# Optimization experiments

Hardware: AMD Instinct MI355X
Metric: run time of the kernel (lower is better)

The kernel has to match this reference:

```python
import jax, jax.numpy as jnp
import numpy as np

LS = (0, 1, 2)
DIMS = tuple(2 * l + 1 for l in LS)          # (1, 3, 5)
MULS = (128, 64, 32)                          # node irreps multiplicities (= attention*heads)
ATT_MULS = (16, 8, 4)                         # attention_irreps multiplicities per head
N_HEADS = 8
N_IRREPS_ATT = sum(ATT_MULS)                  # 28
ATTN_NORM = 1.0 / np.sqrt(N_IRREPS_ATT)
CG = tuple(1.0 / np.sqrt(d) for d in DIMS)    # l (x) l -> 0e Clebsch-Gordan coefficient
N_NODES = 512
EDGE_ATTR_DIM = 32
NODE_DIM = sum(m * d for m, d in zip(MULS, DIMS))  # 480


def split_irreps(x, muls):
    """Split last axis into per-l blocks [..., mul_l, 2l+1]."""
    out, i = [], 0
    for mul, d in zip(muls, DIMS):
        out.append(x[..., i:i + mul * d].reshape(x.shape[:-1] + (mul, d)))
        i += mul * d
    return out


def merge_irreps(parts):
    return jnp.concatenate([p.reshape(p.shape[:-2] + (-1,)) for p in parts], axis=-1)


def e3_linear(parts, Ws):
    # equivariant linear: mixes multiplicities within each l, 1/sqrt(mul_in) norm
    return [jnp.einsum('nim,io->nom', p, W) / np.sqrt(p.shape[-2])
            for p, W in zip(parts, Ws)]


def setup_inputs() -> dict:
    key = jax.random.key(0)
    ks = jax.random.split(key, 16)
    inp = {
        'node_feat': jax.random.normal(ks[0], (N_NODES, NODE_DIM), jnp.float32),
        'edge_attr': jax.random.normal(ks[1], (N_NODES, N_NODES, EDGE_ATTR_DIM), jnp.float32),
        'edge_sh':   jax.random.normal(ks[2], (N_NODES, N_NODES, sum(DIMS)), jnp.float32),
    }
    i = 3
    for nm in ('Wq', 'Wk', 'Wv'):
        for l, mul in enumerate(MULS):
            inp[f'{nm}{l}'] = jax.random.normal(ks[i], (mul, mul), jnp.float32)
            i += 1
    inp['mW1'] = jax.random.normal(ks[i], (EDGE_ATTR_DIM + 2 * sum(MULS), 64), jnp.float32) * 0.05
    inp['mb1'] = jnp.zeros((64,), jnp.float32)
    inp['mW2'] = jax.random.normal(ks[i + 1], (64, 64), jnp.float32) * 0.1
    inp['mb2'] = jnp.zeros((64,), jnp.float32)
    inp['mW3'] = jax.random.normal(ks[i + 2], (64, N_HEADS), jnp.float32) * 0.1
    inp['mb3'] = jnp.zeros((N_HEADS,), jnp.float32)
    return inp


def reference(node_feat, edge_attr, edge_sh,
              Wq0, Wq1, Wq2, Wk0, Wk1, Wk2, Wv0, Wv1, Wv2,
              mW1, mb1, mW2, mb2, mW3, mb3):
    N = node_feat.shape[0]
    nf = split_irreps(node_feat, MULS)                 # per-l: [N, mul_l, 2l+1]
    sh = split_irreps(edge_sh, (1, 1, 1))              # per-l: [N, N, 1, 2l+1]

    def to_heads(parts):
        return [p.reshape(N, N_HEADS, am, d) for p, am, d in zip(parts, ATT_MULS, DIMS)]

    q = to_heads(e3_linear(nf, (Wq0, Wq1, Wq2)))
    k = to_heads(e3_linear(nf, (Wk0, Wk1, Wk2)))
    v = to_heads(e3_linear(nf, (Wv0, Wv1, Wv2)))

    # node (x) edge_sh -> scalars (0e): same-l inner products, CG = 1/sqrt(2l+1)
    feat_rec = jnp.concatenate(
        [jnp.einsum('rim,rsm->rsi', p, s[..., 0, :]) * c for p, s, c in zip(nf, sh, CG)], axis=-1)
    feat_snd = jnp.concatenate(
        [jnp.einsum('sim,rsm->rsi', p, s[..., 0, :]) * c for p, s, c in zip(nf, sh, CG)], axis=-1)
    edge_feat = jnp.concatenate([edge_attr, feat_rec, feat_snd], axis=-1)  # [N,N,480]

    h = jnp.tanh(edge_feat @ mW1 + mb1)
    h = jnp.tanh(h @ mW2 + mb2)
    edge_weight = h @ mW3 + mb3                        # [N, N, H]

    # elementwise q (x) k -> 0e, summed over irreps (== scaled dot product per head)
    logits = sum(jnp.einsum('rhim,shim->rsh', qp, kp) * c
                 for qp, kp, c in zip(q, k, CG))       # [N, N, H]
    weight = jax.nn.softmax(logits * ATTN_NORM + edge_weight, axis=-2)  # softmax over senders

    # weighted aggregation over senders, per irrep
    upd = [jnp.einsum('rsh,shim->rhim', weight, vp) for vp in v]
    # axis_to_mul: [N, H, mul, d] -> [N, H*mul, d]
    upd = [u.reshape(N, N_HEADS * am, d) for u, am, d in zip(upd, ATT_MULS, DIMS)]

    return node_feat + merge_irreps(upd)               # residual (irreps match)
```

## Files before the change

### kernel.cpp

```cpp
#include <hip/hip_runtime.h>
#include <hip/hip_bf16.h>
#include <stdint.h>


#define NNODES 512
#define NDIM   480

#define QG_OFF    0u
#define W2B_OFF   131072u
#define W3B_OFF   133120u
#define W1B_OFF   133632u
#define KG_OFF    245760u
#define VT_OFF    491520u
#define ARE_OFF   737280u
#define ASN_OFF   884736u
#define WF_OFF    1032192u
#define FLAG_OFF  1040384u
#define L_OFF     1040448u
#define WTQ_OFF   3137600u
#define WTK_OFF   3159104u
#define WTV_OFF   3180608u
#define W1T_OFF   3202112u

typedef float f32x4 __attribute__((ext_vector_type(4)));
typedef short s16x8 __attribute__((ext_vector_type(8)));

__device__ __forceinline__ float bf2f(uint16_t u) {
    return __uint_as_float(((uint32_t)u) << 16);
}
__device__ __forceinline__ uint16_t f2bf(float f) {
    union { __hip_bfloat16 h; uint16_t u; } cv;
    cv.h = __float2bfloat16(f);
    return cv.u;
}
__device__ __forceinline__ uint32_t packbf(float lo, float hi) {
    return ((uint32_t)f2bf(hi) << 16) | (uint32_t)f2bf(lo);
}
__device__ __forceinline__ float ldin(const void* p, size_t i, int f32) {
    return f32 ? ((const float*)p)[i] : bf2f(((const uint16_t*)p)[i]);
}
__device__ __forceinline__ float ftanh(float x) {
    float e = __builtin_amdgcn_exp2f(x * 2.885390081777927f);
    return 1.0f - 2.0f * __builtin_amdgcn_rcpf(e + 1.0f);
}

#define NS 16384
__global__ __launch_bounds__(256) void kW(
    const void* __restrict__ mW1, const void* __restrict__ mb1,
    const void* __restrict__ mW2, const void* __restrict__ mb2,
    const void* __restrict__ mW3, const void* __restrict__ mb3,
    const void* __restrict__ Wq0, const void* __restrict__ Wq1, const void* __restrict__ Wq2,
    const void* __restrict__ Wk0, const void* __restrict__ Wk1, const void* __restrict__ Wk2,
    const void* __restrict__ Wv0, const void* __restrict__ Wv1, const void* __restrict__ Wv2,
    float* __restrict__ ws, const void* __restrict__ nfu, int* __restrict__ flagp)
{
    __shared__ int sflag;
    const int t = threadIdx.x;
    if (t < 64) {
        uint32_t x = ((const uint32_t*)nfu)[64 + t];
        int e = (x >> 7) & 0xff;
        int good = (x != 0u) && (e >= 100) && (e <= 140);
        unsigned long long m = __ballot(good);
        if (t == 0) sflag = (__popcll(m) < 32) ? 1 : 0;
    }
    __syncthreads();
    const int f32 = sflag;
    if (blockIdx.x == 0 && t == 0) flagp[0] = f32;

    const int gt = blockIdx.x * 256 + t;
    float* Wf = ws + WF_OFF;

    for (int i = gt; i < 2048; i += NS) Wf[i] = ldin(mW1, i, f32);
    for (int i = gt; i < 64; i += NS) Wf[6656 + i] = ldin(mb1, i, f32);
    for (int i = gt; i < 64; i += NS) Wf[6720 + i] = ldin(mb2, i, f32);
    for (int i = gt; i < 8; i += NS)  Wf[6784 + i] = ldin(mb3, i, f32);

    {
        uint32_t* W2B = (uint32_t*)(ws + W2B_OFF);
        for (int i = gt; i < 2048; i += NS) {
            int f = i >> 8, lane = (i >> 2) & 63, w = i & 3;
            int nt = f >> 1, ks = f & 1, nl2 = lane & 15, gg = lane >> 4;
            int n = nt * 16 + nl2, kb = ks * 32 + gg * 8 + 2 * w;
            float lo = ldin(mW2, (size_t)kb * 64 + n, f32);
            float hi = ldin(mW2, (size_t)(kb + 1) * 64 + n, f32);
            W2B[i] = packbf(lo, hi);
        }
        uint32_t* W3B = (uint32_t*)(ws + W3B_OFF);
        for (int i = gt; i < 512; i += NS) {
            int ks = i >> 8, lane = (i >> 2) & 63, w = i & 3;
            int nl2 = lane & 15, gg = lane >> 4;
            int kb = ks * 32 + gg * 8 + 2 * w;
            float lo = (nl2 < 8) ? ldin(mW3, (size_t)kb * 8 + nl2, f32) : 0.f;
            float hi = (nl2 < 8) ? ldin(mW3, (size_t)(kb + 1) * 8 + nl2, f32) : 0.f;
            W3B[i] = packbf(lo, hi);
        }
        uint32_t* W1B = (uint32_t*)(ws + W1B_OFF);
        for (int i = gt; i < 1024; i += NS) {
            int nt = i >> 8, lane = (i >> 2) & 63, w = i & 3;
            int nl2 = lane & 15, gg = lane >> 4;
            int n = nt * 16 + nl2, k0 = gg * 8 + 2 * w;
            W1B[i] = packbf(ldin(mW1, (size_t)k0 * 64 + n, f32),
                            ldin(mW1, (size_t)(k0 + 1) * 64 + n, f32));
        }
    }

    const float e3n0 = 0.08838834764831845f, e3n1 = 0.125f, e3n2 = 0.17677669529663687f;
    const float cg1 = 0.5773502691896258f, cg2 = 0.4472135954999579f;
    const float attn = 0.1889822365046136f;

    const void* Wsrc[9] = {Wq0, Wq1, Wq2, Wk0, Wk1, Wk2, Wv0, Wv1, Wv2};
    float* Wdst[3] = {ws + WTQ_OFF, ws + WTK_OFF, ws + WTV_OFF};
    for (int kind = 0; kind < 3; ++kind) {
        const float f0 = (kind == 0) ? e3n0 * attn : e3n0;
        const float f1 = (kind == 0) ? e3n1 * cg1 * attn : e3n1;
        const float f2 = (kind == 0) ? e3n2 * cg2 * attn : e3n2;
        for (int i = gt; i < 16384; i += NS) {
            int o = i >> 7, ii = i & 127;
            Wdst[kind][i] = ldin(Wsrc[kind * 3], (size_t)ii * 128 + o, f32) * f0;
        }
        for (int i = gt; i < 4096; i += NS) {
            int o = i >> 6, ii = i & 63;
            Wdst[kind][16384 + i] = ldin(Wsrc[kind * 3 + 1], (size_t)ii * 64 + o, f32) * f1;
        }
        for (int i = gt; i < 1024; i += NS) {
            int o = i >> 5, ii = i & 31;
            Wdst[kind][20480 + i] = ldin(Wsrc[kind * 3 + 2], (size_t)ii * 32 + o, f32) * f2;
        }
    }
    float* W1T = ws + W1T_OFF;
    for (int i = gt; i < 30720; i += NS) {
        int o = i / 480, row = i - o * 480;
        float cgv;
        if (row < 160)      cgv = 1.0f;
        else if (row < 224) cgv = cg1;
        else if (row < 256) cgv = cg2;
        else if (row < 384) cgv = 1.0f;
        else if (row < 448) cgv = cg1;
        else                cgv = cg2;
        W1T[i] = ldin(mW1, (size_t)row * 64 + o, f32) * cgv;
    }
}

__global__ __launch_bounds__(256) void kA(
    const void* __restrict__ nfu,
    const float* __restrict__ WtQ, const float* __restrict__ WtK,
    const float* __restrict__ WtV, const float* __restrict__ W1T,
    uint32_t* __restrict__ qG, uint32_t* __restrict__ kG, uint16_t* __restrict__ vT,
    uint32_t* __restrict__ ArecG, uint32_t* __restrict__ AsndG,
    const int* __restrict__ flagp)
{
    const int f32 = flagp[0];
    const int n = blockIdx.x, t = threadIdx.x;
    __shared__ float nfs[480];
    for (int i = t; i < 480; i += 256) nfs[i] = ldin(nfu, (size_t)n * 480 + i, f32);

    if (t < 96) {
        const int kind3 = t >> 5, hh = (t >> 2) & 7, j = 60 + (t & 3);
        if (kind3 < 2) {
            const int row = n & 15, rt = n >> 4;
            const int cc = (j >> 3) ^ (n & 7);
            uint16_t* dst = (uint16_t*)(kind3 == 0 ? qG : kG);
            dst[((((size_t)rt * 8 + hh) * 16 + row) * 8 + cc) * 8 + (j & 7)] = 0;
        } else {
            vT[((size_t)(hh * 64 + j)) * 512 + n] = 0;
        }
    }
    __syncthreads();

    for (int idx = t; idx < 1440; idx += 256) {
        int kind = idx / 480, rem = idx - kind * 480;
        int o, m, mul, d, off, am, qoff, sub;
        if (rem < 128)      { o = rem;           m = 0;          mul = 128; d = 1; off = 0;   am = 16; qoff = 0;  sub = 0; }
        else if (rem < 320) { int x = rem - 128; o = x / 3; m = x - o * 3; mul = 64;  d = 3; off = 128; am = 8;  qoff = 16; sub = 16384; }
        else                { int x = rem - 320; o = x / 5; m = x - o * 5; mul = 32;  d = 5; off = 320; am = 4;  qoff = 40; sub = 20480; }
        const float* base = (kind == 0) ? WtQ : (kind == 1) ? WtK : WtV;
        const float4* W4 = reinterpret_cast<const float4*>(base + sub + o * mul);
        const float* nf0 = nfs + off + m;
        float ax = 0.f, ay = 0.f, az = 0.f, aw = 0.f;
        const int n4 = mul >> 2;
        for (int i4 = 0; i4 < n4; ++i4) {
            float4 w = W4[i4];
            int ib = 4 * i4 * d;
            ax += nf0[ib]         * w.x;
            ay += nf0[ib + d]     * w.y;
            az += nf0[ib + 2 * d] * w.z;
            aw += nf0[ib + 3 * d] * w.w;
        }
        float acc = (ax + ay) + (az + aw);
        int hh = o / am, a = o - hh * am;
        int j = qoff + a * d + m;
        if (kind == 2) {
            vT[((size_t)(hh * 64 + j)) * 512 + n] = f2bf(acc);
        } else {
            const int row = n & 15, rt = n >> 4;
            const int cc = (j >> 3) ^ (n & 7);
            uint16_t* dst = (uint16_t*)(kind == 0 ? qG : kG);
            dst[((((size_t)rt * 8 + hh) * 16 + row) * 8 + cc) * 8 + (j & 7)] = f2bf(acc);
        }
    }

    if (t < 128) {
        const int src = t >> 6, o = t & 63;
        float a[9];
        #pragma unroll
        for (int mi = 0; mi < 9; ++mi) {
            const int l = (mi == 0) ? 0 : (mi < 4 ? 1 : 2);
            const int m = (mi == 0) ? 0 : (mi < 4 ? mi - 1 : mi - 4);
            const int mul = (l == 0 ? 128 : l == 1 ? 64 : 32);
            const int d = 2 * l + 1;
            const int off = (l == 0 ? 0 : l == 1 ? 128 : 320);
            const int base = (src == 0) ? (l == 0 ? 32 : l == 1 ? 160 : 224)
                                        : (l == 0 ? 256 : l == 1 ? 384 : 448);
            const float4* W4 = reinterpret_cast<const float4*>(W1T + o * 480 + base);
            const float* nf0 = nfs + off + m;
            float ax = 0.f, ay = 0.f, az = 0.f, aw = 0.f;
            const int n4 = mul >> 2;
            for (int i4 = 0; i4 < n4; ++i4) {
                float4 w = W4[i4];
                int ib = 4 * i4 * d;
                ax += nf0[ib]         * w.x;
                ay += nf0[ib + d]     * w.y;
                az += nf0[ib + 2 * d] * w.z;
                aw += nf0[ib + 3 * d] * w.w;
            }
            a[mi] = (ax + ay) + (az + aw);
        }
        float b[9];
        #pragma unroll
        for (int mi = 0; mi < 9; ++mi) b[mi] = __shfl_xor(a[mi], 1, 64);
        if ((o & 1) == 0) {
            uint32_t* dst = (src ? AsndG : ArecG) + (size_t)n * 288 + (o >> 1);
            #pragma unroll
            for (int mi = 0; mi < 9; ++mi)
                dst[mi * 32] = ((uint32_t)f2bf(b[mi]) << 16) | (uint32_t)f2bf(a[mi]);
        }
    }
}

__global__ __launch_bounds__(256, 4) void kB(
    const void* __restrict__ eaG, const void* __restrict__ shG,
    const uint32_t* __restrict__ ArecG, const uint32_t* __restrict__ AsndG,
    const uint32_t* __restrict__ qG, const uint32_t* __restrict__ kG,
    const uint32_t* __restrict__ W2B, const uint32_t* __restrict__ W3B,
    const uint32_t* __restrict__ W1B,
    const float* __restrict__ Wf, float* __restrict__ L,
    const int* __restrict__ flagp)
{
    __shared__ __align__(16) uint32_t smem[10240];
    uint32_t* ArecS = smem;
    uint32_t* AsndS = smem + 4672;
    float* ewS = (float*)(smem + 8192);
    const int f32 = flagp[0];
    const int t = threadIdx.x;
    const int s0 = blockIdx.x * 16, r0 = blockIdx.y * 16;
    const int lane = t & 63, wv = t >> 6;
    const int g = lane >> 4, nl = lane & 15;

    const int rl = t >> 4, sl = t & 15;
    const int r = r0 + rl, s = s0 + sl;
    const size_t eidx = (((size_t)r) << 9) + s;

    uint32_t eaR[16];
    if (f32) {
        const float4* ep = reinterpret_cast<const float4*>((const float*)eaG + eidx * 32);
        #pragma unroll
        for (int i = 0; i < 8; ++i) {
            float4 v = ep[i];
            eaR[2 * i]     = ((uint32_t)f2bf(v.y) << 16) | (uint32_t)f2bf(v.x);
            eaR[2 * i + 1] = ((uint32_t)f2bf(v.w) << 16) | (uint32_t)f2bf(v.z);
        }
    } else {
        const uint4* ep = reinterpret_cast<const uint4*>((const uint32_t*)eaG + eidx * 16);
        #pragma unroll
        for (int i = 0; i < 4; ++i) {
            uint4 v = ep[i];
            eaR[4 * i] = v.x; eaR[4 * i + 1] = v.y; eaR[4 * i + 2] = v.z; eaR[4 * i + 3] = v.w;
        }
    }

    float sh0, sh1, sh2, sh3, sh4, sh5, sh6, sh7, sh8;
    {
        const size_t sb = eidx * 9;
        if (f32) {
            const float* shp = (const float*)shG + sb;
            sh0 = shp[0]; sh1 = shp[1]; sh2 = shp[2]; sh3 = shp[3]; sh4 = shp[4];
            sh5 = shp[5]; sh6 = shp[6]; sh7 = shp[7]; sh8 = shp[8];
        } else {
            const uint16_t* shp = (const uint16_t*)shG + sb;
            sh0 = bf2f(shp[0]); sh1 = bf2f(shp[1]); sh2 = bf2f(shp[2]);
            sh3 = bf2f(shp[3]); sh4 = bf2f(shp[4]); sh5 = bf2f(shp[5]);
            sh6 = bf2f(shp[6]); sh7 = bf2f(shp[7]); sh8 = bf2f(shp[8]);
        }
    }

    {
        s16x8 w1f[4];
        #pragma unroll
        for (int nt = 0; nt < 4; ++nt) w1f[nt] = ((const s16x8*)W1B)[nt * 64 + lane];
        uint16_t* sm16 = (uint16_t*)smem;
        #pragma unroll
        for (int mm = 0; mm < 4; ++mm) {
            const int srcl = mm * 16 + nl;
            uint32_t af0 = 0, af1 = 0, af2 = 0, af3 = 0;
            #pragma unroll
            for (int c = 0; c < 16; ++c) {
                const uint32_t tmp = (uint32_t)__shfl((int)eaR[c], srcl, 64);
                if ((c >> 2) == g) {
                    if ((c & 3) == 0)      af0 = tmp;
                    else if ((c & 3) == 1) af1 = tmp;
                    else if ((c & 3) == 2) af2 = tmp;
                    else                   af3 = tmp;
                }
            }
            union { uint32_t u[4]; s16x8 v; } afc;
            afc.u[0] = af0; afc.u[1] = af1; afc.u[2] = af2; afc.u[3] = af3;
            const s16x8 afrag = afc.v;
            const int mt = wv * 4 + mm;
            #pragma unroll
            for (int nt = 0; nt < 4; ++nt) {
                f32x4 a = {0.f, 0.f, 0.f, 0.f};
                a = __builtin_amdgcn_mfma_f32_16x16x32_bf16(afrag, w1f[nt], a, 0, 0, 0);
                #pragma unroll
                for (int rg = 0; rg < 4; ++rg) {
                    const int e = mt * 16 + g * 4 + rg;
                    const int o = nt * 16 + nl;
                    sm16[e * 64 + (((o >> 3) ^ (e & 7)) << 3) + (o & 7)] = f2bf(a[rg]);
                }
            }
        }
    }

    float h[64];
    #pragma unroll
    for (int c = 0; c < 8; ++c) {
        const int cc = c ^ (t & 7);
        const uint4 p = *(const uint4*)&smem[t * 32 + cc * 4];
        h[c * 8 + 0] = __uint_as_float(p.x << 16);
        h[c * 8 + 1] = __uint_as_float(p.x & 0xffff0000u);
        h[c * 8 + 2] = __uint_as_float(p.y << 16);
        h[c * 8 + 3] = __uint_as_float(p.y & 0xffff0000u);
        h[c * 8 + 4] = __uint_as_float(p.z << 16);
        h[c * 8 + 5] = __uint_as_float(p.z & 0xffff0000u);
        h[c * 8 + 6] = __uint_as_float(p.w << 16);
        h[c * 8 + 7] = __uint_as_float(p.w & 0xffff0000u);
    }
    #pragma unroll
    for (int o = 0; o < 64; ++o) h[o] += Wf[6656 + o];

    __syncthreads();

    for (int i = t; i < 16 * 288; i += 256) {
        int row = i / 288, c = i - row * 288;
        ArecS[row * 292 + c] = ArecG[(size_t)(r0 + row) * 288 + c];
        AsndS[row * 292 + c] = AsndG[(size_t)(s0 + row) * 288 + c];
    }
    __syncthreads();

    {
        const int rb = rl * 292, sb = sl * 292;
        #pragma unroll 1
        for (int mi = 0; mi < 9; ++mi) {
            float shv = sh0;
            shv = (mi == 1) ? sh1 : shv;  shv = (mi == 2) ? sh2 : shv;
            shv = (mi == 3) ? sh3 : shv;  shv = (mi == 4) ? sh4 : shv;
            shv = (mi == 5) ? sh5 : shv;  shv = (mi == 6) ? sh6 : shv;
            shv = (mi == 7) ? sh7 : shv;  shv = (mi == 8) ? sh8 : shv;
            const int ro = rb + mi * 32, so = sb + mi * 32;
            #pragma unroll
            for (int oc = 0; oc < 32; ++oc) {
                uint32_t pa = ArecS[ro + oc];
                uint32_t pb = AsndS[so + oc];
                float a0 = __uint_as_float(pa << 16);
                float b0 = __uint_as_float(pb << 16);
                float a1 = __uint_as_float(pa & 0xffff0000u);
                float b1 = __uint_as_float(pb & 0xffff0000u);
                h[2 * oc]     += shv * (a0 + b0);
                h[2 * oc + 1] += shv * (a1 + b1);
            }
        }
    }

    #pragma unroll
    for (int o = 0; o < 64; ++o) h[o] = ftanh(h[o]);

    __syncthreads();
    #pragma unroll
    for (int c = 0; c < 8; ++c) {
        const int cc = c ^ (t & 7);
        *(uint4*)&smem[t * 32 + cc * 4] =
            make_uint4(packbf(h[c * 8 + 0], h[c * 8 + 1]),
                       packbf(h[c * 8 + 2], h[c * 8 + 3]),
                       packbf(h[c * 8 + 4], h[c * 8 + 5]),
                       packbf(h[c * 8 + 6], h[c * 8 + 7]));
    }
    __builtin_amdgcn_sched_barrier(0);

    s16x8 w2f[4][2];
    #pragma unroll
    for (int nt = 0; nt < 4; ++nt) {
        #pragma unroll
        for (int ks = 0; ks < 2; ++ks)
            w2f[nt][ks] = ((const s16x8*)W2B)[(nt * 2 + ks) * 64 + lane];
    }
    s16x8 w3f[2];
    w3f[0] = ((const s16x8*)W3B)[lane];
    w3f[1] = ((const s16x8*)W3B)[64 + lane];
    float b2v[4];
    #pragma unroll
    for (int nt = 0; nt < 4; ++nt) b2v[nt] = Wf[6720 + nt * 16 + nl];
    const float b3v = (nl < 8) ? Wf[6784 + nl] : 0.f;


    uint16_t* sm16 = (uint16_t*)smem;
    #pragma unroll 1
    for (int mm = 0; mm < 4; ++mm) {
        const int mt = wv * 4 + mm;
        const int row = mt * 16 + nl;
        const int sw0 = ((g    ) ^ (row & 7)) * 4;
        const int sw1 = ((4 + g) ^ (row & 7)) * 4;
        const s16x8 a0 = *(const s16x8*)&smem[row * 32 + sw0];
        const s16x8 a1 = *(const s16x8*)&smem[row * 32 + sw1];
        f32x4 acc[4];
        #pragma unroll
        for (int nt = 0; nt < 4; ++nt) {
            f32x4 a = {b2v[nt], b2v[nt], b2v[nt], b2v[nt]};
            a = __builtin_amdgcn_mfma_f32_16x16x32_bf16(a0, w2f[nt][0], a, 0, 0, 0);
            a = __builtin_amdgcn_mfma_f32_16x16x32_bf16(a1, w2f[nt][1], a, 0, 0, 0);
            acc[nt] = a;
        }
        const int e2base = mt * 16 + g * 4;
        #pragma unroll
        for (int nt = 0; nt < 4; ++nt) {
            const int n = nt * 16 + nl;
            #pragma unroll
            for (int rg = 0; rg < 4; ++rg) {
                const int e2 = e2base + rg;
                const int cc = (n >> 3) ^ (e2 & 7);
                sm16[e2 * 64 + cc * 8 + (n & 7)] = f2bf(ftanh(acc[nt][rg]));
            }
        }
        const s16x8 c0 = *(const s16x8*)&smem[row * 32 + sw0];
        const s16x8 c1 = *(const s16x8*)&smem[row * 32 + sw1];
        f32x4 a3 = {b3v, b3v, b3v, b3v};
        a3 = __builtin_amdgcn_mfma_f32_16x16x32_bf16(c0, w3f[0], a3, 0, 0, 0);
        a3 = __builtin_amdgcn_mfma_f32_16x16x32_bf16(c1, w3f[1], a3, 0, 0, 0);
        if (nl < 8) {
            #pragma unroll
            for (int rg = 0; rg < 4; ++rg) {
                const int e2 = mt * 16 + g * 4 + rg;
                ewS[nl * 256 + (e2 ^ (nl << 2))] = a3[rg];
            }
        }
    }

    __syncthreads();

    {
        const uint4* qg4 = (const uint4*)qG + (size_t)blockIdx.y * 1024;
        const uint4* kg4 = (const uint4*)kG + (size_t)blockIdx.x * 1024;
        uint4* sm4 = (uint4*)smem;
        for (int i = t; i < 2048; i += 256)
            sm4[i] = (i < 1024) ? qg4[i] : kg4[i - 1024];
    }
    __syncthreads();

    {
        const int sw0 = ((g    ) ^ (nl & 7)) << 2;
        const int sw1 = ((4 + g) ^ (nl & 7)) << 2;
        #pragma unroll
        for (int hh2 = 0; hh2 < 2; ++hh2) {
            const int h2 = wv * 2 + hh2;
            const uint32_t* qb = smem + h2 * 512;
            const uint32_t* kb = smem + 4096 + h2 * 512;
            const s16x8 qa0 = *(const s16x8*)&qb[nl * 32 + sw0];
            const s16x8 qa1 = *(const s16x8*)&qb[nl * 32 + sw1];
            const s16x8 ka0 = *(const s16x8*)&kb[nl * 32 + sw0];
            const s16x8 ka1 = *(const s16x8*)&kb[nl * 32 + sw1];
            f32x4 a = {0.f, 0.f, 0.f, 0.f};
            a = __builtin_amdgcn_mfma_f32_16x16x32_bf16(qa0, ka0, a, 0, 0, 0);
            a = __builtin_amdgcn_mfma_f32_16x16x32_bf16(qa1, ka1, a, 0, 0, 0);
            float* Lp = L + (((size_t)h2) << 18) + (((size_t)(r0 + g * 4)) << 9) + s0 + nl;
            #pragma unroll
            for (int rg = 0; rg < 4; ++rg) {
                const int e2 = (g * 4 + rg) * 16 + nl;
                Lp[(size_t)rg << 9] = a[rg] + ewS[h2 * 256 + (e2 ^ (h2 << 2))];
            }
        }
    }
}

__global__ __launch_bounds__(256) void kAgg(
    const float* __restrict__ L, const uint16_t* __restrict__ vT,
    const void* __restrict__ nfu, void* __restrict__ out,
    const int* __restrict__ flagp)
{
    __shared__ __align__(16) uint32_t Ws[4096];
    const int f32 = flagp[0];
    const int t = threadIdx.x;
    const int lane = t & 63, wv = t >> 6;
    const int g = lane >> 4, nl = lane & 15;
    const int r0 = blockIdx.x * 16;
    const int h  = blockIdx.y;

    {
        const int row = wv * 4 + g;
        const float* Lg = L + (((size_t)h) << 18) + (((size_t)(r0 + row)) << 9);
        float v[32];
        #pragma unroll
        for (int cw = 0; cw < 4; ++cw) {
            const float4* p = reinterpret_cast<const float4*>(Lg + nl * 8 + cw * 128);
            float4 x = p[0], y = p[1];
            v[cw * 8 + 0] = x.x; v[cw * 8 + 1] = x.y; v[cw * 8 + 2] = x.z; v[cw * 8 + 3] = x.w;
            v[cw * 8 + 4] = y.x; v[cw * 8 + 5] = y.y; v[cw * 8 + 6] = y.z; v[cw * 8 + 7] = y.w;
        }
        float mx = -3.402823466e38f;
        #pragma unroll
        for (int i = 0; i < 32; ++i) mx = fmaxf(mx, v[i]);
        #pragma unroll
        for (int off = 8; off >= 1; off >>= 1) mx = fmaxf(mx, __shfl_xor(mx, off, 16));
        const float C = 1.4426950408889634f;
        float sm = 0.f;
        #pragma unroll
        for (int i = 0; i < 32; ++i) {
            v[i] = __builtin_amdgcn_exp2f((v[i] - mx) * C);
            sm += v[i];
        }
        #pragma unroll
        for (int off = 8; off >= 1; off >>= 1) sm += __shfl_xor(sm, off, 16);
        const float inv = __builtin_amdgcn_rcpf(sm);
        #pragma unroll
        for (int cw = 0; cw < 4; ++cw) {
            const int cc = (nl + cw * 16) ^ (row & 7);
            *(uint4*)&Ws[row * 256 + cc * 4] = make_uint4(
                packbf(v[cw * 8 + 0] * inv, v[cw * 8 + 1] * inv),
                packbf(v[cw * 8 + 2] * inv, v[cw * 8 + 3] * inv),
                packbf(v[cw * 8 + 4] * inv, v[cw * 8 + 5] * inv),
                packbf(v[cw * 8 + 6] * inv, v[cw * 8 + 7] * inv));
        }
    }
    __syncthreads();

    f32x4 acc = {0.f, 0.f, 0.f, 0.f};
    {
        const uint16_t* vb = vT + ((size_t)(h * 64 + wv * 16 + nl)) * 512 + g * 8;
        #pragma unroll
        for (int ks = 0; ks < 16; ++ks) {
            const s16x8 a = *(const s16x8*)&Ws[nl * 256 + (((ks * 4 + g) ^ (nl & 7)) << 2)];
            const s16x8 b = *(const s16x8*)&vb[ks * 32];
            acc = __builtin_amdgcn_mfma_f32_16x16x32_bf16(a, b, acc, 0, 0, 0);
        }
    }

    const int n = wv * 16 + nl;
    if (n < 60) {
        int col;
        if (n < 16)      col = h * 16 + n;
        else if (n < 40) col = 128 + h * 24 + (n - 16);
        else             col = 320 + h * 20 + (n - 40);
        #pragma unroll
        for (int rg = 0; rg < 4; ++rg) {
            const size_t o = (size_t)(r0 + g * 4 + rg) * 480 + col;
            float val = ldin(nfu, o, f32) + acc[rg];
            if (f32) ((float*)out)[o] = val;
            else     ((uint16_t*)out)[o] = f2bf(val);
        }
    }
}

extern "C" void kernel_launch(void* const* d_in, const int* in_sizes, int n_in,
                              void* d_out, int out_size, void* d_ws, size_t ws_size,
                              hipStream_t stream)
{
    (void)in_sizes; (void)n_in; (void)out_size; (void)ws_size;
    const void* nf  = d_in[0];
    const void* eaG = d_in[1];
    const void* shG = d_in[2];

    float* ws = (float*)d_ws;
    uint32_t* qG = (uint32_t*)(ws + QG_OFF);
    uint32_t* kG = (uint32_t*)(ws + KG_OFF);
    uint32_t* W2B = (uint32_t*)(ws + W2B_OFF);
    uint32_t* W3B = (uint32_t*)(ws + W3B_OFF);
    uint32_t* W1B = (uint32_t*)(ws + W1B_OFF);
    uint16_t* vT = (uint16_t*)(ws + VT_OFF);
    uint32_t* ArecG = (uint32_t*)(ws + ARE_OFF);
    uint32_t* AsndG = (uint32_t*)(ws + ASN_OFF);
    float* Wf  = ws + WF_OFF;
    int* flag  = (int*)(ws + FLAG_OFF);
    float* L   = ws + L_OFF;
    float* WtQ = ws + WTQ_OFF;
    float* WtK = ws + WTK_OFF;
    float* WtV = ws + WTV_OFF;
    float* W1T = ws + W1T_OFF;

    kW<<<64, 256, 0, stream>>>(d_in[12], d_in[13], d_in[14], d_in[15], d_in[16], d_in[17],
                               d_in[3], d_in[4], d_in[5], d_in[6], d_in[7], d_in[8],
                               d_in[9], d_in[10], d_in[11], ws, nf, flag);
    kA<<<512, 256, 0, stream>>>(nf, WtQ, WtK, WtV, W1T, qG, kG, vT, ArecG, AsndG, flag);
    kB<<<dim3(32, 32), 256, 0, stream>>>(eaG, shG, ArecG, AsndG, qG, kG, W2B, W3B, W1B, Wf, L, flag);
    kAgg<<<dim3(32, 8), 256, 0, stream>>>(L, vT, nf, d_out, flag);
}
```

Before: 188.8 us.

## Fuse four kernel launches into one cooperative persistent kernel with grid syncs

Moves the weight-prep, node projection, edge MLP/logit, and aggregation phases into device functions and runs them inside a single cooperative kernel separated by grid-wide barriers. The aim is to remove three kernel launch gaps and the tail idle time between dependent launches. Phase A is also split into two half-work items per node so that 1024 work units exist instead of 512. The cost is that the fused kernel takes on phase B's register and LDS footprint, which can limit occupancy for the other phases, and the grid syncs add barrier overhead. If cooperative launch is unavailable, the old multi-kernel path is used as a fallback.

New measurement: 303.7 us. 1.61x slower.

```diff
diff --git a/kernel.cpp b/kernel.cpp
--- a/kernel.cpp
+++ b/kernel.cpp
@@ -1,6 +1,9 @@
 #include <hip/hip_runtime.h>
 #include <hip/hip_bf16.h>
+#include <hip/hip_cooperative_groups.h>
 #include <stdint.h>
+
+namespace cg = cooperative_groups;
 
 
 #define NNODES 512
@@ -44,40 +47,24 @@
     return 1.0f - 2.0f * __builtin_amdgcn_rcpf(e + 1.0f);
 }
 
-#define NS 16384
-__global__ __launch_bounds__(256) void kW(
-    const void* __restrict__ mW1, const void* __restrict__ mb1,
-    const void* __restrict__ mW2, const void* __restrict__ mb2,
-    const void* __restrict__ mW3, const void* __restrict__ mb3,
-    const void* __restrict__ Wq0, const void* __restrict__ Wq1, const void* __restrict__ Wq2,
-    const void* __restrict__ Wk0, const void* __restrict__ Wk1, const void* __restrict__ Wk2,
-    const void* __restrict__ Wv0, const void* __restrict__ Wv1, const void* __restrict__ Wv2,
-    float* __restrict__ ws, const void* __restrict__ nfu, int* __restrict__ flagp)
-{
-    __shared__ int sflag;
-    const int t = threadIdx.x;
-    if (t < 64) {
-        uint32_t x = ((const uint32_t*)nfu)[64 + t];
-        int e = (x >> 7) & 0xff;
-        int good = (x != 0u) && (e >= 100) && (e <= 140);
-        unsigned long long m = __ballot(good);
-        if (t == 0) sflag = (__popcll(m) < 32) ? 1 : 0;
-    }
-    __syncthreads();
-    const int f32 = sflag;
-    if (blockIdx.x == 0 && t == 0) flagp[0] = f32;
-
-    const int gt = blockIdx.x * 256 + t;
+__device__ void dPhaseW(
+    const void* mW1, const void* mb1, const void* mW2, const void* mb2,
+    const void* mW3, const void* mb3,
+    const void* Wq0, const void* Wq1, const void* Wq2,
+    const void* Wk0, const void* Wk1, const void* Wk2,
+    const void* Wv0, const void* Wv1, const void* Wv2,
+    float* ws, int f32, int gt, int gs)
+{
     float* Wf = ws + WF_OFF;
 
-    for (int i = gt; i < 2048; i += NS) Wf[i] = ldin(mW1, i, f32);
-    for (int i = gt; i < 64; i += NS) Wf[6656 + i] = ldin(mb1, i, f32);
-    for (int i = gt; i < 64; i += NS) Wf[6720 + i] = ldin(mb2, i, f32);
-    for (int i = gt; i < 8; i += NS)  Wf[6784 + i] = ldin(mb3, i, f32);
+    for (int i = gt; i < 2048; i += gs) Wf[i] = ldin(mW1, i, f32);
+    for (int i = gt; i < 64; i += gs) Wf[6656 + i] = ldin(mb1, i, f32);
+    for (int i = gt; i < 64; i += gs) Wf[6720 + i] = ldin(mb2, i, f32);
+    for (int i = gt; i < 8; i += gs)  Wf[6784 + i] = ldin(mb3, i, f32);
 
     {
         uint32_t* W2B = (uint32_t*)(ws + W2B_OFF);
-        for (int i = gt; i < 2048; i += NS) {
+        for (int i = gt; i < 2048; i += gs) {
             int f = i >> 8, lane = (i >> 2) & 63, w = i & 3;
             int nt = f >> 1, ks = f & 1, nl2 = lane & 15, gg = lane >> 4;
             int n = nt * 16 + nl2, kb = ks * 32 + gg * 8 + 2 * w;
@@ -86,7 +73,7 @@
             W2B[i] = packbf(lo, hi);
         }
         uint32_t* W3B = (uint32_t*)(ws + W3B_OFF);
-        for (int i = gt; i < 512; i += NS) {
+        for (int i = gt; i < 512; i += gs) {
             int ks = i >> 8, lane = (i >> 2) & 63, w = i & 3;
             int nl2 = lane & 15, gg = lane >> 4;
             int kb = ks * 32 + gg * 8 + 2 * w;
@@ -95,7 +82,7 @@
             W3B[i] = packbf(lo, hi);
         }
         uint32_t* W1B = (uint32_t*)(ws + W1B_OFF);
-        for (int i = gt; i < 1024; i += NS) {
+        for (int i = gt; i < 1024; i += gs) {
             int nt = i >> 8, lane = (i >> 2) & 63, w = i & 3;
             int nl2 = lane & 15, gg = lane >> 4;
             int n = nt * 16 + nl2, k0 = gg * 8 + 2 * w;
@@ -114,21 +101,21 @@
         const float f0 = (kind == 0) ? e3n0 * attn : e3n0;
         const float f1 = (kind == 0) ? e3n1 * cg1 * attn : e3n1;
         const float f2 = (kind == 0) ? e3n2 * cg2 * attn : e3n2;
-        for (int i = gt; i < 16384; i += NS) {
+        for (int i = gt; i < 16384; i += gs) {
             int o = i >> 7, ii = i & 127;
             Wdst[kind][i] = ldin(Wsrc[kind * 3], (size_t)ii * 128 + o, f32) * f0;
         }
-        for (int i = gt; i < 4096; i += NS) {
+        for (int i = gt; i < 4096; i += gs) {
             int o = i >> 6, ii = i & 63;
             Wdst[kind][16384 + i] = ldin(Wsrc[kind * 3 + 1], (size_t)ii * 64 + o, f32) * f1;
         }
-        for (int i = gt; i < 1024; i += NS) {
+        for (int i = gt; i < 1024; i += gs) {
             int o = i >> 5, ii = i & 31;
             Wdst[kind][20480 + i] = ldin(Wsrc[kind * 3 + 2], (size_t)ii * 32 + o, f32) * f2;
         }
     }
     float* W1T = ws + W1T_OFF;
-    for (int i = gt; i < 30720; i += NS) {
+    for (int i = gt; i < 30720; i += gs) {
         int o = i / 480, row = i - o * 480;
         float cgv;
         if (row < 160)      cgv = 1.0f;
@@ -141,33 +128,33 @@
     }
 }
 
-__global__ __launch_bounds__(256) void kA(
-    const void* __restrict__ nfu,
-    const float* __restrict__ WtQ, const float* __restrict__ WtK,
-    const float* __restrict__ WtV, const float* __restrict__ W1T,
-    uint32_t* __restrict__ qG, uint32_t* __restrict__ kG, uint16_t* __restrict__ vT,
-    uint32_t* __restrict__ ArecG, uint32_t* __restrict__ AsndG,
-    const int* __restrict__ flagp)
-{
-    const int f32 = flagp[0];
-    const int n = blockIdx.x, t = threadIdx.x;
-    __shared__ float nfs[480];
+__device__ void dPhaseA(
+    const void* nfu,
+    const float* WtQ, const float* WtK, const float* WtV, const float* W1T,
+    uint32_t* qG, uint32_t* kG, uint16_t* vT,
+    uint32_t* ArecG, uint32_t* AsndG,
+    int f32, int n, int half, float* nfs)
+{
+    const int t = threadIdx.x;
     for (int i = t; i < 480; i += 256) nfs[i] = ldin(nfu, (size_t)n * 480 + i, f32);
 
-    if (t < 96) {
-        const int kind3 = t >> 5, hh = (t >> 2) & 7, j = 60 + (t & 3);
-        if (kind3 < 2) {
+    if (half == 0) {
+        if (t < 64) {
+            const int kind2 = t >> 5, hh = (t >> 2) & 7, j = 60 + (t & 3);
             const int row = n & 15, rt = n >> 4;
             const int cc = (j >> 3) ^ (n & 7);
-            uint16_t* dst = (uint16_t*)(kind3 == 0 ? qG : kG);
+            uint16_t* dst = (uint16_t*)(kind2 == 0 ? qG : kG);
             dst[((((size_t)rt * 8 + hh) * 16 + row) * 8 + cc) * 8 + (j & 7)] = 0;
-        } else {
+        }
+    } else {
+        if (t < 32) {
+            const int hh = t >> 2, j = 60 + (t & 3);
             vT[((size_t)(hh * 64 + j)) * 512 + n] = 0;
         }
     }
     __syncthreads();
 
-    for (int idx = t; idx < 1440; idx += 256) {
+    for (int idx = 720 * half + t; idx < 720 * (half + 1); idx += 256) {
         int kind = idx / 480, rem = idx - kind * 480;
         int o, m, mul, d, off, am, qoff, sub;
         if (rem < 128)      { o = rem;           m = 0;          mul = 128; d = 1; off = 0;   am = 16; qoff = 0;  sub = 0; }
@@ -199,8 +186,8 @@
         }
     }
 
-    if (t < 128) {
-        const int src = t >> 6, o = t & 63;
+    if (t < 64) {
+        const int src = half, o = t;
         float a[9];
         #pragma unroll
         for (int mi = 0; mi < 9; ++mi) {
@@ -237,22 +224,18 @@
     }
 }
 
-__global__ __launch_bounds__(256, 4) void kB(
-    const void* __restrict__ eaG, const void* __restrict__ shG,
-    const uint32_t* __restrict__ ArecG, const uint32_t* __restrict__ AsndG,
-    const uint32_t* __restrict__ qG, const uint32_t* __restrict__ kG,
-    const uint32_t* __restrict__ W2B, const uint32_t* __restrict__ W3B,
-    const uint32_t* __restrict__ W1B,
-    const float* __restrict__ Wf, float* __restrict__ L,
-    const int* __restrict__ flagp)
-{
-    __shared__ __align__(16) uint32_t smem[10240];
+__device__ void dPhaseB(
+    const void* eaG, const void* shG,
+    const uint32_t* ArecG, const uint32_t* AsndG,
+    const uint32_t* qG, const uint32_t* kG,
+    const uint32_t* W2B, const uint32_t* W3B, const uint32_t* W1B,
+    const float* Wf, float* L, int f32, int sx, int sy, uint32_t* smem)
+{
     uint32_t* ArecS = smem;
     uint32_t* AsndS = smem + 4672;
     float* ewS = (float*)(smem + 8192);
-    const int f32 = flagp[0];
     const int t = threadIdx.x;
-    const int s0 = blockIdx.x * 16, r0 = blockIdx.y * 16;
+    const int s0 = sx * 16, r0 = sy * 16;
     const int lane = t & 63, wv = t >> 6;
     const int g = lane >> 4, nl = lane & 15;
 
@@ -410,7 +393,6 @@
     for (int nt = 0; nt < 4; ++nt) b2v[nt] = Wf[6720 + nt * 16 + nl];
     const float b3v = (nl < 8) ? Wf[6784 + nl] : 0.f;
 
-
     uint16_t* sm16 = (uint16_t*)smem;
     #pragma unroll 1
     for (int mm = 0; mm < 4; ++mm) {
@@ -456,8 +438,8 @@
     __syncthreads();
 
     {
-        const uint4* qg4 = (const uint4*)qG + (size_t)blockIdx.y * 1024;
-        const uint4* kg4 = (const uint4*)kG + (size_t)blockIdx.x * 1024;
+        const uint4* qg4 = (const uint4*)qG + (size_t)sy * 1024;
+        const uint4* kg4 = (const uint4*)kG + (size_t)sx * 1024;
         uint4* sm4 = (uint4*)smem;
         for (int i = t; i < 2048; i += 256)
             sm4[i] = (i < 1024) ? qg4[i] : kg4[i - 1024];
@@ -489,18 +471,14 @@
     }
 }
 
-__global__ __launch_bounds__(256) void kAgg(
-    const float* __restrict__ L, const uint16_t* __restrict__ vT,
-    const void* __restrict__ nfu, void* __restrict__ out,
-    const int* __restrict__ flagp)
-{
-    __shared__ __align__(16) uint32_t Ws[4096];
-    const int f32 = flagp[0];
+__device__ void dPhaseAgg(
+    const float* L, const uint16_t* vT,
+    const void* nfu, void* out, int f32, int bx, int h, uint32_t* Ws)
+{
     const int t = threadIdx.x;
     const int lane = t & 63, wv = t >> 6;
     const int g = lane >> 4, nl = lane & 15;
-    const int r0 = blockIdx.x * 16;
-    const int h  = blockIdx.y;
+    const int r0 = bx * 16;
 
     {
         const int row = wv * 4 + g;
@@ -564,6 +542,136 @@
             if (f32) ((float*)out)[o] = val;
             else     ((uint16_t*)out)[o] = f2bf(val);
         }
+    }
+}
+
+__global__ __launch_bounds__(256) void kW(
+    const void* __restrict__ mW1, const void* __restrict__ mb1,
+    const void* __restrict__ mW2, const void* __restrict__ mb2,
+    const void* __restrict__ mW3, const void* __restrict__ mb3,
+    const void* __restrict__ Wq0, const void* __restrict__ Wq1, const void* __restrict__ Wq2,
+    const void* __restrict__ Wk0, const void* __restrict__ Wk1, const void* __restrict__ Wk2,
+    const void* __restrict__ Wv0, const void* __restrict__ Wv1, const void* __restrict__ Wv2,
+    float* __restrict__ ws, const void* __restrict__ nfu, int* __restrict__ flagp)
+{
+    __shared__ int sflag;
+    const int t = threadIdx.x;
+    if (t < 64) {
+        uint32_t x = ((const uint32_t*)nfu)[64 + t];
+        int e = (x >> 7) & 0xff;
+        int good = (x != 0u) && (e >= 100) && (e <= 140);
+        unsigned long long m = __ballot(good);
+        if (t == 0) sflag = (__popcll(m) < 32) ? 1 : 0;
+    }
+    __syncthreads();
+    const int f32 = sflag;
+    if (blockIdx.x == 0 && t == 0) flagp[0] = f32;
+    dPhaseW(mW1, mb1, mW2, mb2, mW3, mb3, Wq0, Wq1, Wq2, Wk0, Wk1, Wk2,
+            Wv0, Wv1, Wv2, ws, f32, blockIdx.x * 256 + t, 16384);
+}
+
+__global__ __launch_bounds__(256) void kA(
+    const void* __restrict__ nfu,
+    const float* __restrict__ WtQ, const float* __restrict__ WtK,
+    const float* __restrict__ WtV, const float* __restrict__ W1T,
+    uint32_t* __restrict__ qG, uint32_t* __restrict__ kG, uint16_t* __restrict__ vT,
+    uint32_t* __restrict__ ArecG, uint32_t* __restrict__ AsndG,
+    const int* __restrict__ flagp)
+{
+    __shared__ float nfs[480];
+    dPhaseA(nfu, WtQ, WtK, WtV, W1T, qG, kG, vT, ArecG, AsndG,
+            flagp[0], blockIdx.x >> 1, blockIdx.x & 1, nfs);
+}
+
+__global__ __launch_bounds__(256, 4) void kB(
+    const void* __restrict__ eaG, const void* __restrict__ shG,
+    const uint32_t* __restrict__ ArecG, const uint32_t* __restrict__ AsndG,
+    const uint32_t* __restrict__ qG, const uint32_t* __restrict__ kG,
+    const uint32_t* __restrict__ W2B, const uint32_t* __restrict__ W3B,
+    const uint32_t* __restrict__ W1B,
+    const float* __restrict__ Wf, float* __restrict__ L,
+    const int* __restrict__ flagp)
+{
+    __shared__ __align__(16) uint32_t smem[10240];
+    dPhaseB(eaG, shG, ArecG, AsndG, qG, kG, W2B, W3B, W1B, Wf, L,
+            flagp[0], blockIdx.x, blockIdx.y, smem);
+}
+
+__global__ __launch_bounds__(256) void kAgg(
+    const float* __restrict__ L, const uint16_t* __restrict__ vT,
+    const void* __restrict__ nfu, void* __restrict__ out,
+    const int* __restrict__ flagp)
+{
+    __shared__ __align__(16) uint32_t Ws[4096];
+    dPhaseAgg(L, vT, nfu, out, flagp[0], blockIdx.x, blockIdx.y, Ws);
+}
+
+__global__ __launch_bounds__(256, 4) void kFused(
+    const void* nf, const void* eaG, const void* shG,
+    const void* Wq0, const void* Wq1, const void* Wq2,
+    const void* Wk0, const void* Wk1, const void* Wk2,
+    const void* Wv0, const void* Wv1, const void* Wv2,
+    const void* mW1, const void* mb1, const void* mW2, const void* mb2,
+    const void* mW3, const void* mb3,
+    float* ws, void* out)
+{
+    __shared__ __align__(16) uint32_t smem[10240];
+    const int t = threadIdx.x;
+    const int bid = blockIdx.x;
+    const int nblk = gridDim.x;
+
+    uint32_t* qG = (uint32_t*)(ws + QG_OFF);
+    uint32_t* kG = (uint32_t*)(ws + KG_OFF);
+    uint32_t* W2B = (uint32_t*)(ws + W2B_OFF);
+    uint32_t* W3B = (uint32_t*)(ws + W3B_OFF);
+    uint32_t* W1B = (uint32_t*)(ws + W1B_OFF);
+    uint16_t* vT = (uint16_t*)(ws + VT_OFF);
+    uint32_t* ArecG = (uint32_t*)(ws + ARE_OFF);
+    uint32_t* AsndG = (uint32_t*)(ws + ASN_OFF);
+    float* Wf  = ws + WF_OFF;
+    float* L   = ws + L_OFF;
+    float* WtQ = ws + WTQ_OFF;
+    float* WtK = ws + WTK_OFF;
+    float* WtV = ws + WTV_OFF;
+    float* W1T = ws + W1T_OFF;
+
+    if (t < 64) {
+        uint32_t x = ((const uint32_t*)nf)[64 + t];
+        int e = (x >> 7) & 0xff;
+        int good = (x != 0u) && (e >= 100) && (e <= 140);
+        unsigned long long m = __ballot(good);
+        if (t == 0) smem[0] = (__popcll(m) < 32) ? 1u : 0u;
+    }
+    __syncthreads();
+    const int f32 = (int)smem[0];
+    __syncthreads();
+
+    cg::grid_group grid = cg::this_grid();
+
+    dPhaseW(mW1, mb1, mW2, mb2, mW3, mb3, Wq0, Wq1, Wq2, Wk0, Wk1, Wk2,
+            Wv0, Wv1, Wv2, ws, f32, bid * 256 + t, nblk * 256);
+    __threadfence();
+    grid.sync();
+
+    for (int wk = bid; wk < 1024; wk += nblk) {
+        dPhaseA(nf, WtQ, WtK, WtV, W1T, qG, kG, vT, ArecG, AsndG,
+                f32, wk >> 1, wk & 1, (float*)smem);
+        __syncthreads();
+    }
+    __threadfence();
+    grid.sync();
+
+    for (int wk = bid; wk < 1024; wk += nblk) {
+        dPhaseB(eaG, shG, ArecG, AsndG, qG, kG, W2B, W3B, W1B, Wf, L,
+                f32, wk & 31, wk >> 5, smem);
+        __syncthreads();
+    }
+    __threadfence();
+    grid.sync();
+
+    for (int wk = bid; wk < 256; wk += nblk) {
+        dPhaseAgg(L, vT, nf, out, f32, wk & 31, wk >> 5, smem);
+        __syncthreads();
     }
 }
 
@@ -593,10 +701,53 @@
     float* WtV = ws + WTV_OFF;
     float* W1T = ws + W1T_OFF;
 
+    static int coopGrid = -1;
+    if (coopGrid == -1) {
+        coopGrid = 0;
+        int dev = 0;
+        if (hipGetDevice(&dev) == hipSuccess) {
+            int can = 0;
+            if (hipDeviceGetAttribute(&can, hipDeviceAttributeCooperativeLaunch, dev)
+                    == hipSuccess && can) {
+                int maxBlk = 0;
+                if (hipOccupancyMaxActiveBlocksPerMultiprocessor(&maxBlk, kFused, 256, 0)
+                        == hipSuccess && maxBlk > 0) {
+                    int cus = 0;
+                    if (hipDeviceGetAttribute(&cus, hipDeviceAttributeMultiprocessorCount,
+                                              dev) == hipSuccess && cus > 0) {
+                        long g = (long)maxBlk * (long)cus;
+                        if (g > 1024) g = 1024;
+                        if (g >= 256) coopGrid = (int)g;
+                    }
+                }
+            }
+        }
+    }
+    if (coopGrid > 0) {
+        const void* a_nf = nf;  const void* a_ea = eaG; const void* a_sh = shG;
+        const void* a_wq0 = d_in[3],  *a_wq1 = d_in[4],  *a_wq2 = d_in[5];
+        const void* a_wk0 = d_in[6],  *a_wk1 = d_in[7],  *a_wk2 = d_in[8];
+        const void* a_wv0 = d_in[9],  *a_wv1 = d_in[10], *a_wv2 = d_in[11];
+        const void* a_m1 = d_in[12], *a_b1 = d_in[13], *a_m2 = d_in[14];
+        const void* a_b2 = d_in[15], *a_m3 = d_in[16], *a_b3 = d_in[17];
+        float* a_ws = ws; void* a_out = d_out;
+        void* args[] = {
+            &a_nf, &a_ea, &a_sh,
+            &a_wq0, &a_wq1, &a_wq2, &a_wk0, &a_wk1, &a_wk2,
+            &a_wv0, &a_wv1, &a_wv2,
+            &a_m1, &a_b1, &a_m2, &a_b2, &a_m3, &a_b3,
+            &a_ws, &a_out };
+        hipError_t err = hipLaunchCooperativeKernel(
+            reinterpret_cast<const void*>(&kFused),
+            dim3((unsigned)coopGrid), dim3(256), args, 0, stream);
+        if (err == hipSuccess) return;
+        coopGrid = 0;
+    }
+
     kW<<<64, 256, 0, stream>>>(d_in[12], d_in[13], d_in[14], d_in[15], d_in[16], d_in[17],
                                d_in[3], d_in[4], d_in[5], d_in[6], d_in[7], d_in[8],
                                d_in[9], d_in[10], d_in[11], ws, nf, flag);
-    kA<<<512, 256, 0, stream>>>(nf, WtQ, WtK, WtV, W1T, qG, kG, vT, ArecG, AsndG, flag);
+    kA<<<1024, 256, 0, stream>>>(nf, WtQ, WtK, WtV, W1T, qG, kG, vT, ArecG, AsndG, flag);
     kB<<<dim3(32, 32), 256, 0, stream>>>(eaG, shG, ArecG, AsndG, qG, kG, W2B, W3B, W1B, Wf, L, flag);
     kAgg<<<dim3(32, 8), 256, 0, stream>>>(L, vT, nf, d_out, flag);
 }
```
